# Kernel tuning notes

Measured on AMD Instinct MI355X. Metric: run time of the kernel, lower is better.

## Reference

```python
import jax, jax.numpy as jnp
import numpy as np

KSIZE, STRIDE, H, W = 7, 4, 128, 128
NH = (H - KSIZE) // STRIDE + 1  # 31
L = NH * NH                     # 961 patches


def conv2d(x, w, b=None, stride=1):
    y = jax.lax.conv_general_dilated(x, w, (stride, stride), 'VALID',
                                     dimension_numbers=('NCHW', 'OIHW', 'NCHW'))
    if b is not None:
        y = y + b[None, :, None, None]
    return y


def refpad(x):
    return jnp.pad(x, ((0, 0), (0, 0), (1, 1), (1, 1)), mode='reflect')


def unfold(x, k, s):
    # torch.nn.Unfold equivalent, returned as (B, C, k, k, L)
    B, C, Hh, Ww = x.shape
    nh = (Hh - k) // s + 1
    nw = (Ww - k) // s + 1
    hi = (jnp.arange(nh) * s)[:, None] + jnp.arange(k)  # (nh, k)
    wi = (jnp.arange(nw) * s)[:, None] + jnp.arange(k)  # (nw, k)
    p = x[:, :, hi]            # (B, C, nh, k, W)
    p = p[:, :, :, :, wi]      # (B, C, nh, k, nw, k)
    p = p.transpose(0, 1, 3, 5, 2, 4).reshape(B, C, k, k, nh * nw)
    return p


def fold(patches, Hh, Ww, k, s):
    # patches: (B, nh, nw, C, k, k); overlap-add like torch.nn.functional.fold
    B, nh, nw, C = patches.shape[0], patches.shape[1], patches.shape[2], patches.shape[3]
    hi = (jnp.arange(nh) * s)[:, None] + jnp.arange(k)  # (nh, k)
    wi = (jnp.arange(nw) * s)[:, None] + jnp.arange(k)  # (nw, k)
    H_idx = hi[:, None, :, None]  # (nh, 1, k, 1)
    W_idx = wi[None, :, None, :]  # (1, nw, 1, k)
    vals = patches.transpose(0, 3, 1, 2, 4, 5)  # (B, C, nh, nw, k, k)
    out = jnp.zeros((B, C, Hh, Ww), patches.dtype)
    return out.at[:, :, H_idx, W_idx].add(vals)


def setup_inputs() -> dict:
    key = jax.random.key(0)
    ks = jax.random.split(key, 16)
    Cin, Ci = 32, 16            # in_channels, inter_channels
    F_in = KSIZE * KSIZE * Ci   # 784
    F_out = F_in // 4           # 196
    s = 0.05
    d = {
        'x':       jax.random.normal(ks[0], (8, Cin, H, W), jnp.float32),
        'g_w':     jax.random.normal(ks[1], (Ci, Cin, 3, 3), jnp.float32) * s,
        'g_b':     jax.random.normal(ks[2], (Ci,), jnp.float32) * s,
        'w_w':     jax.random.normal(ks[3], (Ci, Cin, 3, 3), jnp.float32) * s,
        'w_b':     jax.random.normal(ks[4], (Ci,), jnp.float32) * s,
        'theta_w': jax.random.normal(ks[5], (Cin, Ci, 1, 1), jnp.float32) * s,
        'theta_b': jax.random.normal(ks[6], (Cin,), jnp.float32) * s,
        'fc1_w':   jax.random.normal(ks[7], (F_out, F_in), jnp.float32) * s,
        'fc1_b':   jax.random.normal(ks[8], (F_out,), jnp.float32) * s,
        'mconv_w': jax.random.normal(ks[9], (L, L), jnp.float32) * s,
        'mconv_b': jax.random.normal(ks[10], (L,), jnp.float32) * s,
        'mfc_w':   jax.random.normal(ks[11], (L, L), jnp.float32) * s,
        'mfc_b':   jax.random.normal(ks[12], (L,), jnp.float32) * s,
        'c1_w':    jax.random.normal(ks[13], (Cin // 2, Cin, 3, 3), jnp.float32) * s,
        'c2_w':    jax.random.normal(ks[14], (Cin, Cin // 2, 1, 1), jnp.float32) * s,
    }
    return d


def reference(x, g_w, g_b, w_w, w_b, theta_w, theta_b, fc1_w, fc1_b,
              mconv_w, mconv_b, mfc_w, mfc_b, c1_w, c2_w):
    residual = x
    x1 = conv2d(refpad(x), g_w, g_b)        # (B, Ci, H, W)
    x2 = conv2d(refpad(x), w_w, w_b)        # (B, Ci, H, W)
    x3 = conv2d(x1, theta_w, theta_b)       # (B, Cin, H, W)
    B = x.shape[0]
    Cin = x.shape[1]

    p6 = unfold(x1, KSIZE, STRIDE).transpose(0, 4, 1, 2, 3).reshape(B, L, -1)   # (B,L,Ci*49)
    p4 = unfold(x2, KSIZE, STRIDE).transpose(0, 4, 1, 2, 3).reshape(B, L, -1)   # (B,L,Ci*49)
    p62 = unfold(x3, KSIZE, STRIDE).transpose(0, 4, 1, 2, 3).reshape(B, L, -1)  # (B,L,Cin*49)

    wf = p4 @ fc1_w.T + fc1_b   # (B, L, F)
    xf = p6 @ fc1_w.T + fc1_b   # (B, L, F)
    A = jnp.einsum('blf,bmf->blm', wf, xf)  # (B, L, L)

    # Ti1 (Conv1d k=1 over patch dim) + Ti2 (Linear over patch dim, transposed)
    Ti = jnp.einsum('nc,bcm->bnm', mconv_w + mfc_w, A) + (mconv_b + mfc_b)[None, :, None]
    mask = jax.nn.sigmoid(Ti)
    mask_b = (mask != 0.0).astype(A.dtype)

    scale = wf.shape[-1] ** -0.5
    Am = jax.nn.softmax(A * mask * scale, axis=-1) * mask_b  # (B, L, L)

    y = jnp.einsum('blm,bmf->blf', Am, p62)  # (B, L, Cin*49)
    y = y.reshape(B, NH, NH, Cin, KSIZE, KSIZE)
    out = fold(y, H, W, KSIZE, STRIDE)       # (B, Cin, H, W)

    # BasicBlock: conv3x3(reflect) -> lrelu -> conv1x1 -> lrelu
    o = jax.nn.leaky_relu(conv2d(refpad(out), c1_w), 0.2)
    o = jax.nn.leaky_relu(conv2d(o, c2_w), 0.2)
    out = residual + o
    return Am, out
```

## Files before the change

kernel.cpp:

```cpp
#include <hip/hip_runtime.h>
#include <math.h>

namespace {
constexpr int Bn   = 8;
constexpr int CIN  = 32;
constexpr int CI   = 16;
constexpr int Lp   = 961;
constexpr int FIN  = 784;
constexpr int FOUT = 196;
constexpr int F62  = 1568;

constexpr int FCP  = 224;
constexpr long long FCB = 961LL * FCP;
constexpr int KP   = 992;
constexpr long long WFTB = 196LL * KP;
constexpr long long AMBB = 961LL * KP;
constexpr long long PBTB = 1568LL * KP;
constexpr long long AB   = 961LL * 961;
constexpr int YLD  = 964;
constexpr long long YB = 1568LL * YLD;
constexpr int CK   = 288;
}

typedef __attribute__((ext_vector_type(8))) short short8x;
typedef __attribute__((ext_vector_type(4))) float floatx4;
typedef __attribute__((ext_vector_type(4))) unsigned short ushort4x;

static __device__ __forceinline__ unsigned short f2bf(float x) {
    unsigned int u = __builtin_bit_cast(unsigned int, x);
    u += 0x7fffu + ((u >> 16) & 1u);
    return (unsigned short)(u >> 16);
}
static __device__ __forceinline__ float bf2f(unsigned short h) {
    return __builtin_bit_cast(float, ((unsigned int)h) << 16);
}

__global__ __launch_bounds__(256)
void prep_k(const float* __restrict__ g_w, const float* __restrict__ w_w,
            const float* __restrict__ c1_w,
            unsigned short* __restrict__ cwh, unsigned short* __restrict__ cwl,
            unsigned short* __restrict__ c1h, unsigned short* __restrict__ c1l,
            const float* __restrict__ mconv_w, const float* __restrict__ mfc_w,
            unsigned short* __restrict__ Mwh, unsigned short* __restrict__ Mwl,
            const float* __restrict__ mconv_b, const float* __restrict__ mfc_b,
            float* __restrict__ Mb,
            const float* __restrict__ fc1w,
            unsigned short* __restrict__ Wh, unsigned short* __restrict__ Wl,
            unsigned short* __restrict__ wfTh, unsigned short* __restrict__ wfTl)
{
    int i = blockIdx.x * 256 + threadIdx.x;
    if (i < 9216) {
        int n = i / CK, k = i - n * CK;
        int t = k >> 5, ci = k & 31;
        float v = (n < 16) ? g_w[n * 288 + ci * 9 + t]
                           : w_w[(n - 16) * 288 + ci * 9 + t];
        unsigned short h = f2bf(v);
        cwh[i] = h; cwl[i] = f2bf(v - bf2f(h));
    } else if (i < 13824) {
        int k2 = i - 9216;
        int n = k2 / CK, k = k2 - n * CK;
        int t = k >> 5, ci = k & 31;
        float v = c1_w[n * 288 + ci * 9 + t];
        unsigned short h = f2bf(v);
        c1h[k2] = h; c1l[k2] = f2bf(v - bf2f(h));
    } else if (i < 967136) {
        int k = i - 13824;
        int n = k / KP, c = k - n * KP;
        float v = (c < 961) ? (mconv_w[n * 961 + c] + mfc_w[n * 961 + c]) : 0.0f;
        unsigned short h = f2bf(v);
        Mwh[k] = h; Mwl[k] = f2bf(v - bf2f(h));
    } else if (i < 968097) {
        int k = i - 967136;
        Mb[k] = mconv_b[k] + mfc_b[k];
    } else if (i < 1172897) {
        int k = i - 968097;
        int n = k / 800, kk = k - n * 800;
        float v = (n < 196 && kk < 784) ? fc1w[n * 784 + kk] : 0.0f;
        unsigned short h = f2bf(v);
        Wh[k] = h; Wl[k] = f2bf(v - bf2f(h));
    } else if (i < 1223073) {
        int k = i - 1172897;
        int row = k >> 5, c = k & 31;
        long long pos = (long long)row * KP + 960 + c;
        wfTh[pos] = 0; wfTl[pos] = 0;
    }
}

__global__ __launch_bounds__(256)
void cls_k(const float* __restrict__ src,
           unsigned short* __restrict__ dh_, unsigned short* __restrict__ dl_)
{
    __shared__ float T[4096];
    const int b = blockIdx.x & 7, h = blockIdx.x >> 3;
    const float* sb = src + (size_t)b * 32 * 16384 + h * 128;
    for (int i = threadIdx.x; i < 4096; i += 256) {
        int ci = i >> 7, w = i & 127;
        T[i] = sb[ci * 16384 + w];
    }
    __syncthreads();
    long long obase = ((long long)b * 16384 + (long long)h * 128) * 32;
    for (int i = threadIdx.x; i < 512; i += 256) {
        int w = i >> 2, o = i & 3;
        unsigned short hv[8], lv[8];
        #pragma unroll
        for (int e = 0; e < 8; ++e) {
            float v = T[(o * 8 + e) * 128 + w];
            unsigned short hh = f2bf(v);
            hv[e] = hh; lv[e] = f2bf(v - bf2f(hh));
        }
        *(short8x*)(dh_ + obase + w * 32 + o * 8) = *(short8x*)hv;
        *(short8x*)(dl_ + obase + w * 32 + o * 8) = *(short8x*)lv;
    }
}

template<int NOUT, bool BIAS, bool LEAKY>
__global__ __launch_bounds__(256)
void convcl_k(const unsigned short* __restrict__ Ih,
              const unsigned short* __restrict__ Il,
              const unsigned short* __restrict__ Bh,
              const unsigned short* __restrict__ Bl,
              const float* __restrict__ b1, const float* __restrict__ b2,
              float* __restrict__ o1, float* __restrict__ o2)
{
    __shared__ unsigned short IsH[12480];
    __shared__ unsigned short IsL[12480];

    const int tid = threadIdx.x;
    const int b   = blockIdx.x & 7;
    const int h   = blockIdx.x >> 3;

    for (int i = tid; i < 1560; i += 256) {
        int p = i >> 2, o = i & 3;
        int dh = (p >= 260) ? 2 : (p >= 130) ? 1 : 0;
        int c  = p - dh * 130;
        int gh = h - 1 + dh; gh = (gh < 0) ? 1 : (gh > 127 ? 126 : gh);
        int gw = c - 1;      gw = (gw < 0) ? 1 : (gw > 127 ? 126 : gw);
        long long src = (((long long)b * 16384 + gh * 128 + gw) << 5) + o * 8;
        int dst = p * 32 + ((o ^ ((c >> 1) & 3)) << 3);
        *(short8x*)&IsH[dst] = *(const short8x*)(Ih + src);
        *(short8x*)&IsL[dst] = *(const short8x*)(Il + src);
    }
    __syncthreads();

    const int lane = tid & 63;
    const int wv   = tid >> 6;
    const int wm   = wv * 32;
    const int fr   = lane & 15;
    const int kq   = lane >> 4;
    constexpr int NF = NOUT / 16;

    floatx4 acc[2][NF];
    #pragma unroll
    for (int i = 0; i < 2; ++i)
        #pragma unroll
        for (int j = 0; j < NF; ++j)
            acc[i][j] = (floatx4){0.f, 0.f, 0.f, 0.f};

    #pragma unroll
    for (int t = 0; t < 9; ++t) {
        const int dh = t / 3, dw = t % 3;
        short8x bh_[NF], bl_[NF];
        #pragma unroll
        for (int j = 0; j < NF; ++j) {
            int nr = j * 16 + fr;
            bh_[j] = *(const short8x*)(Bh + nr * CK + t * 32 + kq * 8);
            bl_[j] = *(const short8x*)(Bl + nr * CK + t * 32 + kq * 8);
        }
        #pragma unroll
        for (int i = 0; i < 2; ++i) {
            int col = wm + i * 16 + fr + dw;
            int off = (dh * 130 + col) * 32 + ((kq ^ ((col >> 1) & 3)) << 3);
            short8x ah = *(const short8x*)&IsH[off];
            short8x al = *(const short8x*)&IsL[off];
            #pragma unroll
            for (int j = 0; j < NF; ++j) {
                acc[i][j] = __builtin_amdgcn_mfma_f32_16x16x32_bf16(ah, bh_[j], acc[i][j], 0, 0, 0);
                acc[i][j] = __builtin_amdgcn_mfma_f32_16x16x32_bf16(ah, bl_[j], acc[i][j], 0, 0, 0);
                acc[i][j] = __builtin_amdgcn_mfma_f32_16x16x32_bf16(al, bh_[j], acc[i][j], 0, 0, 0);
            }
        }
    }

    #pragma unroll
    for (int j = 0; j < NF; ++j) {
        int n = j * 16 + fr;
        float bnv = 0.0f;
        if constexpr (BIAS) bnv = (n < 16) ? b1[n] : b2[n - 16];
        float* dst;
        if constexpr (NOUT == 32) {
            dst = (n < 16) ? (o1 + (((size_t)b * 16 + n) * 128 + h) * 128)
                           : (o2 + (((size_t)b * 16 + (n - 16)) * 128 + h) * 128);
        } else {
            dst = o1 + (((size_t)b * 16 + n) * 128 + h) * 128;
        }
        #pragma unroll
        for (int i = 0; i < 2; ++i) {
            int wb = wm + i * 16 + kq * 4;
            floatx4 ov;
            #pragma unroll
            for (int r = 0; r < 4; ++r) {
                float v = acc[i][j][r] + bnv;
                if constexpr (LEAKY) v = (v >= 0.0f) ? v : 0.2f * v;
                ov[r] = v;
            }
            *(floatx4*)(dst + wb) = ov;
        }
    }
}

template<bool BIAS, bool LEAKY, bool RESID>
__global__ __launch_bounds__(256)
void conv1x1p_k(const float* __restrict__ src, const float* __restrict__ wgt,
                const float* __restrict__ bias, const float* __restrict__ resid,
                float* __restrict__ out)
{
    int idx = blockIdx.x * 256 + threadIdx.x;
    int pix = idx & 16383;
    int b   = idx >> 14;
    const float* sb = src + (size_t)b * CI * 16384 + pix;
    float s[16];
    #pragma unroll
    for (int ci = 0; ci < CI; ++ci) s[ci] = sb[ci * 16384];
    size_t ob = (size_t)b * 32 * 16384 + pix;
    #pragma unroll
    for (int co = 0; co < 32; ++co) {
        const float* wrow = wgt + co * CI;
        float acc = BIAS ? bias[co] : 0.0f;
        #pragma unroll
        for (int ci = 0; ci < CI; ++ci) acc += wrow[ci] * s[ci];
        if constexpr (LEAKY) acc = (acc >= 0.0f) ? acc : 0.2f * acc;
        if constexpr (RESID) acc += resid[ob + (size_t)co * 16384];
        out[ob + (size_t)co * 16384] = acc;
    }
}

__global__ __launch_bounds__(256)
void fcmfma2_k(const float* __restrict__ x1s, const float* __restrict__ x2s,
               const unsigned short* __restrict__ Wh,
               const unsigned short* __restrict__ Wl,
               const float* __restrict__ bias,
               unsigned short* __restrict__ Xfh, unsigned short* __restrict__ Xfl,
               unsigned short* __restrict__ Wfh, unsigned short* __restrict__ Wfl,
               unsigned short* __restrict__ DTh, unsigned short* __restrict__ DTl)
{
    __shared__ unsigned short AsH[64*32], AsL[64*32], BsH[64*32], BsL[64*32];
    const int tid = threadIdx.x;
    const bool wrt = blockIdx.x >= 484;
    const int bid = wrt ? (int)blockIdx.x - 484 : (int)blockIdx.x;
    const float* xsrc = wrt ? x2s : x1s;
    unsigned short* Dh = wrt ? Wfh : Xfh;
    unsigned short* Dl = wrt ? Wfl : Xfl;
    const int tm0 = (bid >> 2) * 64;
    const int tn0 = (bid & 3) * 64;

    const int lr = tid >> 2;
    const int lc = tid & 3;
    const int gm = tm0 + lr;
    const bool mok = gm < 7688;
    int gbase = 0;
    if (mok) {
        int b = gm / 961, pi = gm - b * 961;
        int ih = pi / 31, iw = pi - ih * 31;
        gbase = b * 262144 + ih * 512 + iw * 4;
    }
    const int pc = ((lc ^ ((lr >> 1) & 3))) * 8;
    const unsigned short* Whr = Wh + (tn0 + lr) * 800;
    const unsigned short* Wlr = Wl + (tn0 + lr) * 800;

    const int lane = tid & 63, wv = tid >> 6;
    const int wm = (wv >> 1) * 32, wn = (wv & 1) * 32;
    const int fr = lane & 15, kq = lane >> 4;

    floatx4 acc[2][2];
    #pragma unroll
    for (int i = 0; i < 2; ++i)
        #pragma unroll
        for (int j = 0; j < 2; ++j)
            acc[i][j] = (floatx4){0.f, 0.f, 0.f, 0.f};

    float pv[8];
    short8x pwh, pwl;
    auto loadA = [&](int k0) {
        #pragma unroll
        for (int j = 0; j < 8; ++j) {
            int k = k0 + lc * 8 + j;
            float v = 0.0f;
            if (mok && k < 784) {
                int c  = k / 49, r = k - c * 49;
                int kh = r / 7,  kw = r - kh * 7;
                v = xsrc[gbase + c * 16384 + kh * 128 + kw];
            }
            pv[j] = v;
        }
    };
    auto loadW = [&](int k0) {
        pwh = *(const short8x*)(Whr + k0 + lc * 8);
        pwl = *(const short8x*)(Wlr + k0 + lc * 8);
    };

    loadA(0); loadW(0);
    for (int k0 = 0; k0 < 800; k0 += 32) {
        unsigned short hv[8], lv[8];
        #pragma unroll
        for (int j = 0; j < 8; ++j) {
            unsigned short h = f2bf(pv[j]);
            hv[j] = h; lv[j] = f2bf(pv[j] - bf2f(h));
        }
        *(short8x*)&AsH[lr * 32 + pc] = *(short8x*)hv;
        *(short8x*)&AsL[lr * 32 + pc] = *(short8x*)lv;
        *(short8x*)&BsH[lr * 32 + pc] = pwh;
        *(short8x*)&BsL[lr * 32 + pc] = pwl;
        __syncthreads();
        if (k0 + 32 < 800) { loadA(k0 + 32); loadW(k0 + 32); }
        short8x ah[2], al[2], bh[2], bl[2];
        #pragma unroll
        for (int i = 0; i < 2; ++i) {
            int mr = wm + i * 16 + fr;
            int off = mr * 32 + ((kq ^ ((mr >> 1) & 3)) * 8);
            ah[i] = *(const short8x*)&AsH[off];
            al[i] = *(const short8x*)&AsL[off];
        }
        #pragma unroll
        for (int j = 0; j < 2; ++j) {
            int nr = wn + j * 16 + fr;
            int off = nr * 32 + ((kq ^ ((nr >> 1) & 3)) * 8);
            bh[j] = *(const short8x*)&BsH[off];
            bl[j] = *(const short8x*)&BsL[off];
        }
        #pragma unroll
        for (int i = 0; i < 2; ++i)
            #pragma unroll
            for (int j = 0; j < 2; ++j) {
                acc[i][j] = __builtin_amdgcn_mfma_f32_16x16x32_bf16(ah[i], bh[j], acc[i][j], 0, 0, 0);
                acc[i][j] = __builtin_amdgcn_mfma_f32_16x16x32_bf16(ah[i], bl[j], acc[i][j], 0, 0, 0);
                acc[i][j] = __builtin_amdgcn_mfma_f32_16x16x32_bf16(al[i], bh[j], acc[i][j], 0, 0, 0);
            }
        __syncthreads();
    }

    #pragma unroll
    for (int j = 0; j < 2; ++j) {
        int n = tn0 + wn + j * 16 + fr;
        if (n >= FCP) continue;
        float bn = (n < 196) ? bias[n] : 0.0f;
        #pragma unroll
        for (int i = 0; i < 2; ++i) {
            #pragma unroll
            for (int r = 0; r < 4; ++r) {
                int l = tm0 + wm + i * 16 + kq * 4 + r;
                if (l >= 7688) continue;
                int b = l / 961, pi = l - b * 961;
                float v = (n < 196) ? (acc[i][j][r] + bn) : 0.0f;
                unsigned short h = f2bf(v);
                unsigned short lo = f2bf(v - bf2f(h));
                long long base = (long long)b * FCB + (long long)pi * FCP + n;
                Dh[base] = h;
                Dl[base] = lo;
                if (wrt && n < 196) {
                    long long tb = (long long)b * WFTB + (long long)n * KP + pi;
                    DTh[tb] = h;
                    DTl[tb] = lo;
                }
            }
        }
    }
}

__global__ __launch_bounds__(256)
void w2mfma_k(const unsigned short* __restrict__ Xhi,
              const unsigned short* __restrict__ Xlo,
              const unsigned short* __restrict__ Yhi,
              const unsigned short* __restrict__ Ylo,
              unsigned short* __restrict__ W2h,
              unsigned short* __restrict__ W2l)
{
    __shared__ unsigned short XsH[4096], XsL[4096], YsH[4096], YsL[4096];
    const int b   = blockIdx.x & 7;
    const int t   = blockIdx.x >> 3;
    const int tm0 = (t >> 1) * 128;
    const int tn0 = (t & 1) * 128;
    const unsigned short* Ybh = Yhi + (long long)b * WFTB;
    const unsigned short* Ybl = Ylo + (long long)b * WFTB;
    const int tid = threadIdx.x;

    const int sr  = tid >> 1;
    const int sc0 = (tid & 1) * 2;
    const bool xok = (tm0 + sr) < 961;
    const bool yok = (tn0 + sr) < 196;
    const unsigned short* Xrh = Xhi + (long long)(tm0 + sr) * KP;
    const unsigned short* Xrl = Xlo + (long long)(tm0 + sr) * KP;
    const unsigned short* Yrh = Ybh + (long long)(tn0 + sr) * KP;
    const unsigned short* Yrl = Ybl + (long long)(tn0 + sr) * KP;
    const int swz = (sr >> 1) & 3;

    const int lane = tid & 63;
    const int wv   = tid >> 6;
    const int wm   = (wv >> 1) * 64, wn = (wv & 1) * 64;
    const int fr   = lane & 15;
    const int kq   = lane >> 4;

    floatx4 acc[4][4];
    #pragma unroll
    for (int i = 0; i < 4; ++i)
        #pragma unroll
        for (int j = 0; j < 4; ++j)
            acc[i][j] = (floatx4){0.f, 0.f, 0.f, 0.f};

    const short8x zz = {0,0,0,0,0,0,0,0};
    short8x pxh[2], pxl[2], pyh[2], pyl[2];
    auto loadK = [&](int k0) {
        #pragma unroll
        for (int c = 0; c < 2; ++c) {
            int kc = sc0 + c;
            pxh[c] = xok ? *(const short8x*)(Xrh + k0 + kc * 8) : zz;
            pxl[c] = xok ? *(const short8x*)(Xrl + k0 + kc * 8) : zz;
            pyh[c] = yok ? *(const short8x*)(Yrh + k0 + kc * 8) : zz;
            pyl[c] = yok ? *(const short8x*)(Yrl + k0 + kc * 8) : zz;
        }
    };

    loadK(0);
    for (int k0 = 0; k0 < KP; k0 += 32) {
        #pragma unroll
        for (int c = 0; c < 2; ++c) {
            int pc = (sc0 + c) ^ swz;
            *(short8x*)&XsH[sr * 32 + pc * 8] = pxh[c];
            *(short8x*)&XsL[sr * 32 + pc * 8] = pxl[c];
            *(short8x*)&YsH[sr * 32 + pc * 8] = pyh[c];
            *(short8x*)&YsL[sr * 32 + pc * 8] = pyl[c];
        }
        __syncthreads();
        if (k0 + 32 < KP) loadK(k0 + 32);
        short8x bh[4], bl[4];
        #pragma unroll
        for (int j = 0; j < 4; ++j) {
            int nr = wn + j * 16 + fr;
            int off = nr * 32 + ((kq ^ ((nr >> 1) & 3)) * 8);
            bh[j] = *(const short8x*)&YsH[off];
            bl[j] = *(const short8x*)&YsL[off];
        }
        #pragma unroll
        for (int i = 0; i < 4; ++i) {
            int mr = wm + i * 16 + fr;
            int off = mr * 32 + ((kq ^ ((mr >> 1) & 3)) * 8);
            short8x ah = *(const short8x*)&XsH[off];
            short8x al = *(const short8x*)&XsL[off];
            #pragma unroll
            for (int j = 0; j < 4; ++j) {
                acc[i][j] = __builtin_amdgcn_mfma_f32_16x16x32_bf16(ah, bh[j], acc[i][j], 0, 0, 0);
                acc[i][j] = __builtin_amdgcn_mfma_f32_16x16x32_bf16(ah, bl[j], acc[i][j], 0, 0, 0);
                acc[i][j] = __builtin_amdgcn_mfma_f32_16x16x32_bf16(al, bh[j], acc[i][j], 0, 0, 0);
            }
        }
        __syncthreads();
    }

    unsigned short* Wh2 = W2h + (long long)b * FCB;
    unsigned short* Wl2 = W2l + (long long)b * FCB;
    #pragma unroll
    for (int j = 0; j < 4; ++j) {
        int f = tn0 + wn + j * 16 + fr;
        if (f >= FCP) continue;
        #pragma unroll
        for (int i = 0; i < 4; ++i) {
            int lb = tm0 + wm + i * 16 + kq * 4;
            #pragma unroll
            for (int r = 0; r < 4; ++r) {
                int l = lb + r;
                if (l >= 961) continue;
                float v = acc[i][j][r];
                unsigned short h = f2bf(v);
                long long pos = (long long)l * FCP + f;
                Wh2[pos] = h;
                Wl2[pos] = f2bf(v - bf2f(h));
            }
        }
    }
}

__global__ __launch_bounds__(256, 2)
void atimfma_k(const unsigned short* __restrict__ Wfh,
               const unsigned short* __restrict__ Wfl,
               const unsigned short* __restrict__ W2h,
               const unsigned short* __restrict__ W2l,
               const unsigned short* __restrict__ Xfh,
               const unsigned short* __restrict__ Xfl,
               const float* __restrict__ Mb,
               float* __restrict__ Sout)
{
    const int b   = blockIdx.x & 7;
    const int t   = blockIdx.x >> 3;
    const int tm0 = (t >> 3) * 128;
    const int tn0 = (t & 7) * 128;
    const int tid = threadIdx.x;

    const int lane = tid & 63;
    const int wv   = tid >> 6;
    const int wm   = (wv >> 1) * 64, wn = (wv & 1) * 64;
    const int fr   = lane & 15;
    const int kq   = lane >> 4;

    const long long bb = (long long)b * FCB;
    const unsigned short* A1h = Wfh + bb;
    const unsigned short* A1l = Wfl + bb;
    const unsigned short* A2h = W2h + bb;
    const unsigned short* A2l = W2l + bb;
    const unsigned short* Byh = Xfh + bb;
    const unsigned short* Byl = Xfl + bb;

    int aoff[4], boff[4];
    #pragma unroll
    for (int i = 0; i < 4; ++i) {
        int r = tm0 + wm + i * 16 + fr; if (r > 960) r = 960;
        aoff[i] = r * FCP + kq * 8;
    }
    #pragma unroll
    for (int j = 0; j < 4; ++j) {
        int r = tn0 + wn + j * 16 + fr; if (r > 960) r = 960;
        boff[j] = r * FCP + kq * 8;
    }

    floatx4 accA[4][4], accT[4][4];
    #pragma unroll
    for (int i = 0; i < 4; ++i)
        #pragma unroll
        for (int j = 0; j < 4; ++j) {
            accA[i][j] = (floatx4){0.f, 0.f, 0.f, 0.f};
            accT[i][j] = (floatx4){0.f, 0.f, 0.f, 0.f};
        }

    short8x f1h[2][4], f1l[2][4], f2h[2][4], f2l[2][4], fbh[2][4], fbl[2][4];

    #pragma unroll
    for (int j = 0; j < 4; ++j) {
        fbh[0][j] = *(const short8x*)(Byh + boff[j]);
        fbl[0][j] = *(const short8x*)(Byl + boff[j]);
    }
    #pragma unroll
    for (int i = 0; i < 4; ++i) {
        f1h[0][i] = *(const short8x*)(A1h + aoff[i]);
        f1l[0][i] = *(const short8x*)(A1l + aoff[i]);
        f2h[0][i] = *(const short8x*)(A2h + aoff[i]);
        f2l[0][i] = *(const short8x*)(A2l + aoff[i]);
    }

    #pragma unroll
    for (int ks = 0; ks < 7; ++ks) {
        const int cur = ks & 1, nxt = cur ^ 1;
        if (ks < 6) {
            const int k0 = (ks + 1) * 32;
            #pragma unroll
            for (int j = 0; j < 4; ++j) {
                fbh[nxt][j] = *(const short8x*)(Byh + boff[j] + k0);
                fbl[nxt][j] = *(const short8x*)(Byl + boff[j] + k0);
            }
            #pragma unroll
            for (int i = 0; i < 4; ++i) {
                f1h[nxt][i] = *(const short8x*)(A1h + aoff[i] + k0);
                f1l[nxt][i] = *(const short8x*)(A1l + aoff[i] + k0);
                f2h[nxt][i] = *(const short8x*)(A2h + aoff[i] + k0);
                f2l[nxt][i] = *(const short8x*)(A2l + aoff[i] + k0);
            }
        }
        #pragma unroll
        for (int i = 0; i < 4; ++i) {
            #pragma unroll
            for (int j = 0; j < 4; ++j) {
                accA[i][j] = __builtin_amdgcn_mfma_f32_16x16x32_bf16(f1h[cur][i], fbh[cur][j], accA[i][j], 0, 0, 0);
                accA[i][j] = __builtin_amdgcn_mfma_f32_16x16x32_bf16(f1h[cur][i], fbl[cur][j], accA[i][j], 0, 0, 0);
                accA[i][j] = __builtin_amdgcn_mfma_f32_16x16x32_bf16(f1l[cur][i], fbh[cur][j], accA[i][j], 0, 0, 0);
                accT[i][j] = __builtin_amdgcn_mfma_f32_16x16x32_bf16(f2h[cur][i], fbh[cur][j], accT[i][j], 0, 0, 0);
                accT[i][j] = __builtin_amdgcn_mfma_f32_16x16x32_bf16(f2h[cur][i], fbl[cur][j], accT[i][j], 0, 0, 0);
                accT[i][j] = __builtin_amdgcn_mfma_f32_16x16x32_bf16(f2l[cur][i], fbh[cur][j], accT[i][j], 0, 0, 0);
            }
        }
    }

    const float scale = 0.07142857142857142f;
    float* Sb = Sout + (long long)b * AB;
    #pragma unroll
    for (int j = 0; j < 4; ++j) {
        int m = tn0 + wn + j * 16 + fr;
        if (m >= 961) continue;
        #pragma unroll
        for (int i = 0; i < 4; ++i) {
            int lb = tm0 + wm + i * 16 + kq * 4;
            #pragma unroll
            for (int r = 0; r < 4; ++r) {
                int l = lb + r;
                if (l >= 961) continue;
                float ti = accT[i][j][r] + Mb[l];
                float mask = 1.0f / (1.0f + expf(-ti));
                Sb[(long long)l * 961 + m] = accA[i][j][r] * mask * scale;
            }
        }
    }
}

__global__ __launch_bounds__(256)
void softmax_mask_k(const float* __restrict__ S, float* __restrict__ Am,
                    unsigned short* __restrict__ Amb)
{
    int row = blockIdx.x;
    const float* srow = S + (long long)row * Lp;
    float*       orow = Am + (long long)row * Lp;
    unsigned short* brow = Amb + (long long)row * KP;
    int tid = threadIdx.x;

    float s[4], mb[4];
    float lmax = -INFINITY;
    #pragma unroll
    for (int j = 0; j < 4; ++j) {
        int m = tid + j * 256;
        if (m < Lp) {
            float v = srow[m];
            s[j]  = v;
            mb[j] = (v != 0.0f) ? 1.0f : 0.0f;
            lmax  = fmaxf(lmax, v);
        } else { s[j] = -INFINITY; mb[j] = 0.0f; }
    }
    __shared__ float red[256];
    red[tid] = lmax; __syncthreads();
    #pragma unroll
    for (int off = 128; off > 0; off >>= 1) {
        if (tid < off) red[tid] = fmaxf(red[tid], red[tid + off]);
        __syncthreads();
    }
    float rmax = red[0];
    __syncthreads();

    float e[4];
    float lsum = 0.0f;
    #pragma unroll
    for (int j = 0; j < 4; ++j) {
        int m = tid + j * 256;
        e[j] = (m < Lp) ? expf(s[j] - rmax) : 0.0f;
        lsum += e[j];
    }
    red[tid] = lsum; __syncthreads();
    #pragma unroll
    for (int off = 128; off > 0; off >>= 1) {
        if (tid < off) red[tid] += red[tid + off];
        __syncthreads();
    }
    float inv = 1.0f / red[0];
    #pragma unroll
    for (int j = 0; j < 4; ++j) {
        int m = tid + j * 256;
        if (m < Lp) {
            float v = e[j] * inv * mb[j];
            orow[m] = v;
            brow[m] = f2bf(v);
        } else if (m < KP) {
            brow[m] = 0;
        }
    }
}

__global__ __launch_bounds__(256)
void p62bt_k(const float* __restrict__ x3, unsigned short* __restrict__ out)
{
    int idx = blockIdx.x * 256 + threadIdx.x;
    if (idx >= 8 * 1568 * 124) return;
    int ck = idx % 124;
    int t  = idx / 124;
    int n  = t % 1568;
    int b  = t / 1568;
    int c = n / 49, rr = n - c * 49;
    int kh = rr / 7, kw = rr - kh * 7;
    const float* src = x3 + (long long)b * 524288 + c * 16384 + kh * 128 + kw;
    int k = ck * 8;
    unsigned short v[8];
    #pragma unroll
    for (int j = 0; j < 8; ++j) {
        int kk = k + j;
        if (kk < Lp) {
            int ih = kk / 31, iw = kk - ih * 31;
            v[j] = f2bf(src[ih * 512 + iw * 4]);
        } else v[j] = 0;
    }
    *(short8x*)(out + ((long long)b * 1568 + n) * KP + k) = *(short8x*)v;
}

__global__ __launch_bounds__(256)
void ymfma_k(const unsigned short* __restrict__ Amb,
             const unsigned short* __restrict__ Pbt,
             unsigned short* __restrict__ yT)
{
    __shared__ unsigned short As[128 * 32];
    __shared__ unsigned short Bs[128 * 32];
    const int b   = blockIdx.x & 7;
    const int t   = blockIdx.x >> 3;
    const int tn0 = (t % 13) * 128;
    const int tm0 = (t / 13) * 128;
    const unsigned short* Ab = Amb + (long long)b * AMBB;
    const unsigned short* Bb = Pbt + (long long)b * PBTB;
    const int tid = threadIdx.x;

    const int sr  = tid >> 1;
    const int sc0 = (tid & 1) * 2;
    const bool aok = (tm0 + sr) < Lp;
    const bool bok = (tn0 + sr) < F62;
    const unsigned short* Arow = Ab + (long long)(tm0 + sr) * KP;
    const unsigned short* Brow = Bb + (long long)(tn0 + sr) * KP;
    const int swz = (sr >> 1) & 3;

    const int lane = tid & 63;
    const int wv   = tid >> 6;
    const int wm   = (wv >> 1) * 64, wn = (wv & 1) * 64;
    const int fr   = lane & 15;
    const int kq   = lane >> 4;

    floatx4 acc[4][4];
    #pragma unroll
    for (int i = 0; i < 4; ++i)
        #pragma unroll
        for (int j = 0; j < 4; ++j)
            acc[i][j] = (floatx4){0.f, 0.f, 0.f, 0.f};

    const short8x zz = {0,0,0,0,0,0,0,0};
    short8x pa[2], pb[2];
    auto loadK = [&](int k0) {
        #pragma unroll
        for (int c = 0; c < 2; ++c) {
            int kc = sc0 + c;
            pa[c] = aok ? *(const short8x*)(Arow + k0 + kc * 8) : zz;
            pb[c] = bok ? *(const short8x*)(Brow + k0 + kc * 8) : zz;
        }
    };

    loadK(0);
    for (int k0 = 0; k0 < Lp; k0 += 32) {
        #pragma unroll
        for (int c = 0; c < 2; ++c) {
            int pc = (sc0 + c) ^ swz;
            *(short8x*)&As[sr * 32 + pc * 8] = pa[c];
            *(short8x*)&Bs[sr * 32 + pc * 8] = pb[c];
        }
        __syncthreads();
        if (k0 + 32 < Lp) loadK(k0 + 32);
        short8x af[4], bfr[4];
        #pragma unroll
        for (int i = 0; i < 4; ++i) {
            int mr = wm + i * 16 + fr;
            af[i] = *(const short8x*)&As[mr * 32 + ((kq ^ ((mr >> 1) & 3)) * 8)];
        }
        #pragma unroll
        for (int j = 0; j < 4; ++j) {
            int nr = wn + j * 16 + fr;
            bfr[j] = *(const short8x*)&Bs[nr * 32 + ((kq ^ ((nr >> 1) & 3)) * 8)];
        }
        #pragma unroll
        for (int i = 0; i < 4; ++i)
            #pragma unroll
            for (int j = 0; j < 4; ++j)
                acc[i][j] = __builtin_amdgcn_mfma_f32_16x16x32_bf16(
                                af[i], bfr[j], acc[i][j], 0, 0, 0);
        __syncthreads();
    }

    unsigned short* Yb = yT + (long long)b * YB;
    #pragma unroll
    for (int j = 0; j < 4; ++j) {
        int n = tn0 + wn + j * 16 + fr;
        if (n >= F62) continue;
        unsigned short* Yr = Yb + (long long)n * YLD;
        #pragma unroll
        for (int i = 0; i < 4; ++i) {
            int lb = tm0 + wm + i * 16 + kq * 4;
            if (lb >= Lp) continue;
            ushort4x hv;
            #pragma unroll
            for (int r = 0; r < 4; ++r) hv[r] = f2bf(acc[i][j][r]);
            if (lb + 3 < Lp) {
                *(ushort4x*)(Yr + lb) = hv;
            } else {
                #pragma unroll
                for (int r = 0; r < 4; ++r)
                    if (lb + r < Lp) Yr[lb + r] = hv[r];
            }
        }
    }
}

__global__ __launch_bounds__(256)
void foldg_k(const unsigned short* __restrict__ yT, float* __restrict__ out)
{
    int idx = blockIdx.x * 256 + threadIdx.x;
    int wc = idx & 127;
    int hr = (idx >> 7) & 127;
    int c  = (idx >> 14) & 31;
    int b  = idx >> 19;
    int ih_lo = (hr >= 6) ? ((hr - 3) >> 2) : 0;
    int ih_hi = min(hr >> 2, 30);
    int iw_lo = (wc >= 6) ? ((wc - 3) >> 2) : 0;
    int iw_hi = min(wc >> 2, 30);
    const unsigned short* Yb = yT + (long long)b * YB + (long long)c * 49 * YLD;
    float acc = 0.0f;
    for (int ih = ih_lo; ih <= ih_hi; ++ih) {
        int kh = hr - 4 * ih;
        for (int iw = iw_lo; iw <= iw_hi; ++iw) {
            int kw = wc - 4 * iw;
            acc += bf2f(Yb[(kh * 7 + kw) * YLD + ih * 31 + iw]);
        }
    }
    out[idx] = acc;
}

extern "C" void kernel_launch(void* const* d_in, const int* in_sizes, int n_in,
                              void* d_out, int out_size, void* d_ws, size_t ws_size,
                              hipStream_t stream)
{
    const float* x       = (const float*)d_in[0];
    const float* g_w     = (const float*)d_in[1];
    const float* g_b     = (const float*)d_in[2];
    const float* w_w     = (const float*)d_in[3];
    const float* w_b     = (const float*)d_in[4];
    const float* theta_w = (const float*)d_in[5];
    const float* theta_b = (const float*)d_in[6];
    const float* fc1_w   = (const float*)d_in[7];
    const float* fc1_b   = (const float*)d_in[8];
    const float* mconv_w = (const float*)d_in[9];
    const float* mconv_b = (const float*)d_in[10];
    const float* mfc_w   = (const float*)d_in[11];
    const float* mfc_b   = (const float*)d_in[12];
    const float* c1_w    = (const float*)d_in[13];
    const float* c2_w    = (const float*)d_in[14];

    float* Am_out    = (float*)d_out;
    float* final_out = Am_out + (size_t)Bn * Lp * Lp;

    float* ws = (float*)d_ws;
    float* x1    = ws;
    float* x2    = ws + 2097152;
    float* x3    = ws + 4194304;
    unsigned short* xf_hi = (unsigned short*)(ws + 8388608);
    unsigned short* xf_lo = (unsigned short*)(ws + 9249664);
    unsigned short* wf_hi = (unsigned short*)(ws + 10110720);
    unsigned short* wf_lo = (unsigned short*)(ws + 10971776);
    float* Abuf  = ws + 11832832;
    unsigned short* wfT_hi = (unsigned short*)(ws + 19221000);
    unsigned short* wfT_lo = (unsigned short*)(ws + 19998728);
    unsigned short* W2_hi  = (unsigned short*)(ws + 20776456);
    unsigned short* W2_lo  = (unsigned short*)(ws + 21637512);
    unsigned short* Mw_hi = (unsigned short*)(ws + 26847496);
    unsigned short* Mw_lo = (unsigned short*)(ws + 27324152);
    float* Mb    = ws + 27800808;
    unsigned short* fc1wh = (unsigned short*)(ws + 27801832);
    unsigned short* fc1wl = (unsigned short*)(ws + 27904232);
    unsigned short* cwh = (unsigned short*)(ws + 4194304);
    unsigned short* cwl = cwh + 16384;
    unsigned short* c1h = (unsigned short*)(ws + 28006632);
    unsigned short* c1l = c1h + 8192;
    unsigned short* xclH = (unsigned short*)(ws + 11832832);
    unsigned short* xclL = (unsigned short*)(ws + 13929984);
    unsigned short* Am_bf16 = (unsigned short*)x1;
    unsigned short* p62bT   = (unsigned short*)Abuf;
    unsigned short* yT      = wfT_hi;
    unsigned short* fclH    = xclH;
    unsigned short* fclL    = xclL;

    prep_k<<<4778, 256, 0, stream>>>(
        g_w, w_w, c1_w, cwh, cwl, c1h, c1l,
        mconv_w, mfc_w, Mw_hi, Mw_lo,
        mconv_b, mfc_b, Mb, fc1_w, fc1wh, fc1wl,
        wfT_hi, wfT_lo);

    cls_k<<<1024, 256, 0, stream>>>(x, xclH, xclL);

    convcl_k<32, true, false><<<1024, 256, 0, stream>>>(
        xclH, xclL, cwh, cwl, g_b, w_b, x1, x2);

    conv1x1p_k<true, false, false><<<512, 256, 0, stream>>>(
        x1, theta_w, theta_b, nullptr, x3);

    fcmfma2_k<<<968, 256, 0, stream>>>(
        x1, x2, fc1wh, fc1wl, fc1_b,
        xf_hi, xf_lo, wf_hi, wf_lo, wfT_hi, wfT_lo);

    w2mfma_k<<<128, 256, 0, stream>>>(
        Mw_hi, Mw_lo, wfT_hi, wfT_lo, W2_hi, W2_lo);

    atimfma_k<<<512, 256, 0, stream>>>(
        wf_hi, wf_lo, W2_hi, W2_lo, xf_hi, xf_lo, Mb, Abuf);

    softmax_mask_k<<<7688, 256, 0, stream>>>(Abuf, Am_out, Am_bf16);

    p62bt_k<<<6077, 256, 0, stream>>>(x3, p62bT);

    ymfma_k<<<832, 256, 0, stream>>>(Am_bf16, p62bT, yT);

    foldg_k<<<16384, 256, 0, stream>>>(yT, x3);

    cls_k<<<1024, 256, 0, stream>>>(x3, fclH, fclL);

    convcl_k<16, false, true><<<1024, 256, 0, stream>>>(
        fclH, fclL, c1h, c1l, nullptr, nullptr, x1, nullptr);

    conv1x1p_k<false, true, true><<<512, 256, 0, stream>>>(
        x1, c2_w, nullptr, x, final_out);
}
```

Measured before the change: 474.1 us.

## Emit first conv outputs as channel-last bf16 hi/lo for FC gather

The first 3x3 conv now writes x1/x2 as channel-last split bf16 (hi/lo) through shared memory instead of NCHW fp32. The FC-patch GEMM then gathers 8 contiguous channels per tap with vector loads and skips its per-element float-to-bf16 split, with fc1 weights reordered to tap-major to match. The theta 1x1 conv reads the new layout and rebuilds fp32 from hi+lo. This costs an extra shared-memory staging pass and sync in the conv epilogue.

```diff
diff --git a/kernel.cpp b/kernel.cpp
--- a/kernel.cpp
+++ b/kernel.cpp
@@ -75,7 +75,8 @@
     } else if (i < 1172897) {
         int k = i - 968097;
         int n = k / 800, kk = k - n * 800;
-        float v = (n < 196 && kk < 784) ? fc1w[n * 784 + kk] : 0.0f;
+        int tap = kk >> 4, c = kk & 15;
+        float v = (n < 196 && tap < 49) ? fc1w[n * 784 + c * 49 + tap] : 0.0f;
         unsigned short h = f2bf(v);
         Wh[k] = h; Wl[k] = f2bf(v - bf2f(h));
     } else if (i < 1223073) {
@@ -113,14 +114,16 @@
     }
 }
 
-template<int NOUT, bool BIAS, bool LEAKY>
+template<int NOUT, bool BIAS, bool LEAKY, bool CLOUT>
 __global__ __launch_bounds__(256)
 void convcl_k(const unsigned short* __restrict__ Ih,
               const unsigned short* __restrict__ Il,
               const unsigned short* __restrict__ Bh,
               const unsigned short* __restrict__ Bl,
               const float* __restrict__ b1, const float* __restrict__ b2,
-              float* __restrict__ o1, float* __restrict__ o2)
+              float* __restrict__ o1,
+              unsigned short* __restrict__ o1h, unsigned short* __restrict__ o1l,
+              unsigned short* __restrict__ o2h, unsigned short* __restrict__ o2l)
 {
     __shared__ unsigned short IsH[12480];
     __shared__ unsigned short IsL[12480];
@@ -181,46 +184,88 @@
         }
     }
 
-    #pragma unroll
-    for (int j = 0; j < NF; ++j) {
-        int n = j * 16 + fr;
-        float bnv = 0.0f;
-        if constexpr (BIAS) bnv = (n < 16) ? b1[n] : b2[n - 16];
-        float* dst;
+    if constexpr (CLOUT) {
+        __syncthreads();
+        #pragma unroll
+        for (int j = 0; j < NF; ++j) {
+            int n = j * 16 + fr;
+            float bnv = 0.0f;
+            if constexpr (BIAS) bnv = (n < 16) ? b1[n] : b2[n - 16];
+            #pragma unroll
+            for (int i = 0; i < 2; ++i) {
+                int pb = wm + i * 16 + kq * 4;
+                #pragma unroll
+                for (int r = 0; r < 4; ++r) {
+                    float v = acc[i][j][r] + bnv;
+                    if constexpr (LEAKY) v = (v >= 0.0f) ? v : 0.2f * v;
+                    unsigned short hh = f2bf(v);
+                    IsH[(pb + r) * 32 + n] = hh;
+                    IsL[(pb + r) * 32 + n] = f2bf(v - bf2f(hh));
+                }
+            }
+        }
+        __syncthreads();
+        const int p  = tid >> 1;
+        const int c0 = (tid & 1) * 8;
+        long long base = ((long long)b * 16384 + (long long)h * 128 + p) * 16 + c0;
+        *(short8x*)(o1h + base) = *(short8x*)&IsH[p * 32 + c0];
+        *(short8x*)(o1l + base) = *(short8x*)&IsL[p * 32 + c0];
         if constexpr (NOUT == 32) {
-            dst = (n < 16) ? (o1 + (((size_t)b * 16 + n) * 128 + h) * 128)
-                           : (o2 + (((size_t)b * 16 + (n - 16)) * 128 + h) * 128);
-        } else {
-            dst = o1 + (((size_t)b * 16 + n) * 128 + h) * 128;
-        }
-        #pragma unroll
-        for (int i = 0; i < 2; ++i) {
-            int wb = wm + i * 16 + kq * 4;
-            floatx4 ov;
-            #pragma unroll
-            for (int r = 0; r < 4; ++r) {
-                float v = acc[i][j][r] + bnv;
-                if constexpr (LEAKY) v = (v >= 0.0f) ? v : 0.2f * v;
-                ov[r] = v;
-            }
-            *(floatx4*)(dst + wb) = ov;
-        }
-    }
-}
-
-template<bool BIAS, bool LEAKY, bool RESID>
+            *(short8x*)(o2h + base) = *(short8x*)&IsH[p * 32 + 16 + c0];
+            *(short8x*)(o2l + base) = *(short8x*)&IsL[p * 32 + 16 + c0];
+        }
+    } else {
+        #pragma unroll
+        for (int j = 0; j < NF; ++j) {
+            int n = j * 16 + fr;
+            float bnv = 0.0f;
+            if constexpr (BIAS) bnv = (n < 16) ? b1[n] : b2[n - 16];
+            float* dst = o1 + (((size_t)b * NOUT + n) * 128 + h) * 128;
+            #pragma unroll
+            for (int i = 0; i < 2; ++i) {
+                int wb = wm + i * 16 + kq * 4;
+                floatx4 ov;
+                #pragma unroll
+                for (int r = 0; r < 4; ++r) {
+                    float v = acc[i][j][r] + bnv;
+                    if constexpr (LEAKY) v = (v >= 0.0f) ? v : 0.2f * v;
+                    ov[r] = v;
+                }
+                *(floatx4*)(dst + wb) = ov;
+            }
+        }
+    }
+}
+
+template<bool CLSRC, bool BIAS, bool LEAKY, bool RESID>
 __global__ __launch_bounds__(256)
-void conv1x1p_k(const float* __restrict__ src, const float* __restrict__ wgt,
+void conv1x1p_k(const float* __restrict__ src,
+                const unsigned short* __restrict__ srcH,
+                const unsigned short* __restrict__ srcL,
+                const float* __restrict__ wgt,
                 const float* __restrict__ bias, const float* __restrict__ resid,
                 float* __restrict__ out)
 {
     int idx = blockIdx.x * 256 + threadIdx.x;
     int pix = idx & 16383;
     int b   = idx >> 14;
-    const float* sb = src + (size_t)b * CI * 16384 + pix;
     float s[16];
-    #pragma unroll
-    for (int ci = 0; ci < CI; ++ci) s[ci] = sb[ci * 16384];
+    if constexpr (CLSRC) {
+        long long base = ((long long)b * 16384 + pix) * 16;
+        short8x h0 = *(const short8x*)(srcH + base);
+        short8x h1 = *(const short8x*)(srcH + base + 8);
+        short8x l0 = *(const short8x*)(srcL + base);
+        short8x l1 = *(const short8x*)(srcL + base + 8);
+        #pragma unroll
+        for (int ci = 0; ci < 8; ++ci) {
+            s[ci]     = bf2f((unsigned short)h0[ci]) + bf2f((unsigned short)l0[ci]);
+            s[ci + 8] = bf2f((unsigned short)h1[ci]) + bf2f((unsigned short)l1[ci]);
+        }
+    } else {
+        const float* sb = src + (size_t)b * CI * 16384 + pix;
+        #pragma unroll
+        for (int ci = 0; ci < CI; ++ci) s[ci] = sb[ci * 16384];
+    }
     size_t ob = (size_t)b * 32 * 16384 + pix;
     #pragma unroll
     for (int co = 0; co < 32; ++co) {
@@ -235,7 +280,10 @@
 }
 
 __global__ __launch_bounds__(256)
-void fcmfma2_k(const float* __restrict__ x1s, const float* __restrict__ x2s,
+void fcmfma2_k(const unsigned short* __restrict__ x1h,
+               const unsigned short* __restrict__ x1l,
+               const unsigned short* __restrict__ x2h,
+               const unsigned short* __restrict__ x2l,
                const unsigned short* __restrict__ Wh,
                const unsigned short* __restrict__ Wl,
                const float* __restrict__ bias,
@@ -247,7 +295,8 @@
     const int tid = threadIdx.x;
     const bool wrt = blockIdx.x >= 484;
     const int bid = wrt ? (int)blockIdx.x - 484 : (int)blockIdx.x;
-    const float* xsrc = wrt ? x2s : x1s;
+    const unsigned short* Ah = wrt ? x2h : x1h;
+    const unsigned short* Al = wrt ? x2l : x1l;
     unsigned short* Dh = wrt ? Wfh : Xfh;
     unsigned short* Dl = wrt ? Wfl : Xfl;
     const int tm0 = (bid >> 2) * 64;
@@ -257,12 +306,14 @@
     const int lc = tid & 3;
     const int gm = tm0 + lr;
     const bool mok = gm < 7688;
-    int gbase = 0;
+    int gb16 = 0;
     if (mok) {
         int b = gm / 961, pi = gm - b * 961;
         int ih = pi / 31, iw = pi - ih * 31;
-        gbase = b * 262144 + ih * 512 + iw * 4;
-    }
+        gb16 = (b * 16384 + ih * 512 + iw * 4) * 16;
+    }
+    const int tapAdd = lc >> 1;
+    const int c0a    = (lc & 1) * 8;
     const int pc = ((lc ^ ((lr >> 1) & 3))) * 8;
     const unsigned short* Whr = Wh + (tn0 + lr) * 800;
     const unsigned short* Wlr = Wl + (tn0 + lr) * 800;
@@ -278,20 +329,16 @@
         for (int j = 0; j < 2; ++j)
             acc[i][j] = (floatx4){0.f, 0.f, 0.f, 0.f};
 
-    float pv[8];
-    short8x pwh, pwl;
+    const short8x zz = {0,0,0,0,0,0,0,0};
+    short8x pah, pal, pwh, pwl;
     auto loadA = [&](int k0) {
-        #pragma unroll
-        for (int j = 0; j < 8; ++j) {
-            int k = k0 + lc * 8 + j;
-            float v = 0.0f;
-            if (mok && k < 784) {
-                int c  = k / 49, r = k - c * 49;
-                int kh = r / 7,  kw = r - kh * 7;
-                v = xsrc[gbase + c * 16384 + kh * 128 + kw];
-            }
-            pv[j] = v;
-        }
+        int tap = (k0 >> 4) + tapAdd;
+        if (mok && tap < 49) {
+            int kh = tap / 7, kw = tap - kh * 7;
+            int off = gb16 + kh * 2048 + kw * 16 + c0a;
+            pah = *(const short8x*)(Ah + off);
+            pal = *(const short8x*)(Al + off);
+        } else { pah = zz; pal = zz; }
     };
     auto loadW = [&](int k0) {
         pwh = *(const short8x*)(Whr + k0 + lc * 8);
@@ -300,14 +347,8 @@
 
     loadA(0); loadW(0);
     for (int k0 = 0; k0 < 800; k0 += 32) {
-        unsigned short hv[8], lv[8];
-        #pragma unroll
-        for (int j = 0; j < 8; ++j) {
-            unsigned short h = f2bf(pv[j]);
-            hv[j] = h; lv[j] = f2bf(pv[j] - bf2f(h));
-        }
-        *(short8x*)&AsH[lr * 32 + pc] = *(short8x*)hv;
-        *(short8x*)&AsL[lr * 32 + pc] = *(short8x*)lv;
+        *(short8x*)&AsH[lr * 32 + pc] = pah;
+        *(short8x*)&AsL[lr * 32 + pc] = pal;
         *(short8x*)&BsH[lr * 32 + pc] = pwh;
         *(short8x*)&BsL[lr * 32 + pc] = pwl;
         __syncthreads();
@@ -831,8 +872,11 @@
     float* final_out = Am_out + (size_t)Bn * Lp * Lp;
 
     float* ws = (float*)d_ws;
-    float* x1    = ws;
-    float* x2    = ws + 2097152;
+    unsigned short* x1clH = (unsigned short*)ws;
+    unsigned short* x1clL = (unsigned short*)(ws + 1048576);
+    unsigned short* x2clH = (unsigned short*)(ws + 2097152);
+    unsigned short* x2clL = (unsigned short*)(ws + 3145728);
+    float* x1f   = ws;
     float* x3    = ws + 4194304;
     unsigned short* xf_hi = (unsigned short*)(ws + 8388608);
     unsigned short* xf_lo = (unsigned short*)(ws + 9249664);
@@ -854,7 +898,7 @@
     unsigned short* c1l = c1h + 8192;
     unsigned short* xclH = (unsigned short*)(ws + 11832832);
     unsigned short* xclL = (unsigned short*)(ws + 13929984);
-    unsigned short* Am_bf16 = (unsigned short*)x1;
+    unsigned short* Am_bf16 = (unsigned short*)ws;
     unsigned short* p62bT   = (unsigned short*)Abuf;
     unsigned short* yT      = wfT_hi;
     unsigned short* fclH    = xclH;
@@ -868,14 +912,15 @@
 
     cls_k<<<1024, 256, 0, stream>>>(x, xclH, xclL);
 
-    convcl_k<32, true, false><<<1024, 256, 0, stream>>>(
-        xclH, xclL, cwh, cwl, g_b, w_b, x1, x2);
-
-    conv1x1p_k<true, false, false><<<512, 256, 0, stream>>>(
-        x1, theta_w, theta_b, nullptr, x3);
+    convcl_k<32, true, false, true><<<1024, 256, 0, stream>>>(
+        xclH, xclL, cwh, cwl, g_b, w_b,
+        nullptr, x1clH, x1clL, x2clH, x2clL);
+
+    conv1x1p_k<true, true, false, false><<<512, 256, 0, stream>>>(
+        nullptr, x1clH, x1clL, theta_w, theta_b, nullptr, x3);
 
     fcmfma2_k<<<968, 256, 0, stream>>>(
-        x1, x2, fc1wh, fc1wl, fc1_b,
+        x1clH, x1clL, x2clH, x2clL, fc1wh, fc1wl, fc1_b,
         xf_hi, xf_lo, wf_hi, wf_lo, wfT_hi, wfT_lo);
 
     w2mfma_k<<<128, 256, 0, stream>>>(
@@ -894,9 +939,10 @@
 
     cls_k<<<1024, 256, 0, stream>>>(x3, fclH, fclL);
 
-    convcl_k<16, false, true><<<1024, 256, 0, stream>>>(
-        fclH, fclL, c1h, c1l, nullptr, nullptr, x1, nullptr);
-
-    conv1x1p_k<false, true, true><<<512, 256, 0, stream>>>(
-        x1, c2_w, nullptr, x, final_out);
-}
+    convcl_k<16, false, true, false><<<1024, 256, 0, stream>>>(
+        fclH, fclL, c1h, c1l, nullptr, nullptr,
+        x1f, nullptr, nullptr, nullptr, nullptr);
+
+    conv1x1p_k<false, false, true, true><<<512, 256, 0, stream>>>(
+        x1f, nullptr, nullptr, c2_w, nullptr, x, final_out);
+}
```

Result: faster. 459.4 us (-3.1%).
